# Optimization experiments

Measured on AMD Instinct MI355X. Metric: run time of the kernel, lower is better.

The kernel has to match this reference:

```python
import jax, jax.numpy as jnp
import numpy as np

ERR = 1e-12


def setup_inputs() -> dict:
    key = jax.random.key(0)
    k1, k2, k3 = jax.random.split(key, 3)
    B, H, L, D = 2, 16, 2048, 64
    k = jax.random.normal(k1, (B, H, L, D), dtype=jnp.float32)
    src = jax.random.uniform(k2, (B, H, L), dtype=jnp.float32)
    dest = jax.random.uniform(k3, (B, H, L), dtype=jnp.float32)
    return {"k": k, "src": src, "dest": dest}


def reference(k, src, dest):
    # k: [B,H,L,D], src/dest: [B,H,L]
    L = k.shape[-2]
    s = jnp.sqrt(src + ERR)   # sqrt-scaled source weights
    d = jnp.sqrt(dest + ERR)  # sqrt-scaled destination weights
    # affinity_1[b,h,i,j] = s_i * d_j * (k_i . k_j), fused as (k*s) @ (k*d)^T
    a1 = jnp.einsum("bhid,bhjd->bhij", k * s[..., :, None], k * d[..., :, None])
    # relu then (x+err)^(2/3)  (kernel: exp2(log2(relu(a)+err) * 2/3))
    a3 = jnp.exp2(jnp.log2(jax.nn.relu(a1) + ERR) * (2.0 / 3.0))
    # forward cumulative sum over j, output causally masked to j >= i
    cs = jnp.cumsum(a3, axis=-1)
    idx = jnp.arange(L)
    mask = idx[:, None] <= idx[None, :]  # keep j >= i
    return jnp.where(mask, cs, 0.0)
```

## Files before the change

### kernel.cpp

```cpp
#include <hip/hip_runtime.h>

#define BH   32
#define LSEQ 2048
#define DDIM 64
#define ERRC 1e-12f

typedef __attribute__((ext_vector_type(8)))  short bf16x8;
typedef __attribute__((ext_vector_type(4)))  float floatx4;
typedef __attribute__((ext_vector_type(4)))  unsigned short ushort4v;

__device__ __forceinline__ unsigned short f2bf(float f) {
    unsigned u = __float_as_uint(f);
    u = u + 0x7FFFu + ((u >> 16) & 1u);
    return (unsigned short)(u >> 16);
}

__device__ __forceinline__ bf16x8 pack8s(const float* __restrict__ p, float w) {
    const floatx4* pv = (const floatx4*)p;
    floatx4 x = pv[0], y = pv[1];
    bf16x8 r;
    r[0] = (short)f2bf(x[0] * w); r[1] = (short)f2bf(x[1] * w);
    r[2] = (short)f2bf(x[2] * w); r[3] = (short)f2bf(x[3] * w);
    r[4] = (short)f2bf(y[0] * w); r[5] = (short)f2bf(y[1] * w);
    r[6] = (short)f2bf(y[2] * w); r[7] = (short)f2bf(y[3] * w);
    return r;
}

__global__ __launch_bounds__(256) void prep_scaled(const float* __restrict__ k,
                                                   const float* __restrict__ src,
                                                   const float* __restrict__ dest,
                                                   unsigned short* __restrict__ ks,
                                                   unsigned short* __restrict__ kd) {
    int idx4 = blockIdx.x * 256 + threadIdx.x;
    int row  = idx4 >> 4;
    float s = sqrtf(src[row] + ERRC);
    float d = sqrtf(dest[row] + ERRC);
    floatx4 v = ((const floatx4*)k)[idx4];
    ushort4v os, od;
#pragma unroll
    for (int r = 0; r < 4; ++r) { os[r] = f2bf(v[r] * s); od[r] = f2bf(v[r] * d); }
    ((ushort4v*)ks)[idx4] = os;
    ((ushort4v*)kd)[idx4] = od;
}

template<bool RAW>
__device__ __forceinline__ void load_row16(const void* __restrict__ kp, long base, int row,
                                           int q, const float* __restrict__ w, int bhL,
                                           bf16x8& lo, bf16x8& hi) {
    if (RAW) {
        const float* p = (const float*)kp + base + (long)row * DDIM + q * 8;
        float s = sqrtf(w[bhL + row] + ERRC);
        lo = pack8s(p, s);
        hi = pack8s(p + 32, s);
    } else {
        const unsigned short* p = (const unsigned short*)kp + base + (long)row * DDIM + q * 8;
        lo = *(const bf16x8*)p;
        hi = *(const bf16x8*)(p + 32);
    }
}

template<bool RAW>
__global__ __launch_bounds__(256, 4) void mha_fused4(const void* __restrict__ ka,
                                                     const void* __restrict__ kb,
                                                     const float* __restrict__ src,
                                                     const float* __restrict__ dest,
                                                     float* __restrict__ out) {
    const int tid  = threadIdx.x;
    const int wave = tid >> 6;
    const int lane = tid & 63;
    const int q    = lane >> 4;
    const int l16  = lane & 15;
    const int bh = blockIdx.x & 31;
    const int ib = blockIdx.x >> 5;
    const int i0 = (ib * 4 + wave) * 16;
    const int bhL = bh * LSEQ;
    const long base = (long)bh * LSEQ * DDIM;

    bf16x8 blo, bhi;
    load_row16<RAW>(kb, base, i0 + l16, q, src, bhL, blo, bhi);

    float carry = 0.f;
    const float c23 = 2.0f / 3.0f;

    bf16x8 aLo[4], aHi[4];
#pragma unroll
    for (int t = 0; t < 4; ++t)
        load_row16<RAW>(ka, base, 16 * t + l16, q, dest, bhL, aLo[t], aHi[t]);

    float* orow = out + (long)(bhL + i0 + l16) * LSEQ + q * 4;

    for (int it = 0; it < 32; ++it) {
        const int j0 = it << 6;

        bf16x8 nLo[4], nHi[4];
        const int jn = (it < 31) ? (j0 + 64) : 0;
#pragma unroll
        for (int t = 0; t < 4; ++t)
            load_row16<RAW>(ka, base, jn + 16 * t + l16, q, dest, bhL, nLo[t], nHi[t]);

        floatx4 acc[4];
#pragma unroll
        for (int t = 0; t < 4; ++t) {
            floatx4 z = {0.f, 0.f, 0.f, 0.f};
            z = __builtin_amdgcn_mfma_f32_16x16x32_bf16(aLo[t], blo, z, 0, 0, 0);
            acc[t] = __builtin_amdgcn_mfma_f32_16x16x32_bf16(aHi[t], bhi, z, 0, 0, 0);
        }

        float u[4][4];
#pragma unroll
        for (int t = 0; t < 4; ++t)
#pragma unroll
            for (int r = 0; r < 4; ++r) {
                float v = fmaxf(acc[t][r], 0.f) + ERRC;
                u[t][r] = exp2f(c23 * __log2f(v));
            }

        if (j0 + 64 <= i0) {
            float s = 0.f;
#pragma unroll
            for (int t = 0; t < 4; ++t)
                s += (u[t][0] + u[t][1]) + (u[t][2] + u[t][3]);
            float s1 = s + __shfl_xor(s, 16, 64);
            carry += s1 + __shfl_xor(s1, 32, 64);
            const floatx4 z = {0.f, 0.f, 0.f, 0.f};
#pragma unroll
            for (int t = 0; t < 4; ++t)
                *(floatx4*)(orow + j0 + 16 * t) = z;
        } else {
#pragma unroll
            for (int t = 0; t < 4; ++t) {
                const int jt0 = j0 + 16 * t;
                if (jt0 + 16 <= i0) {
                    float s = (u[t][0] + u[t][1]) + (u[t][2] + u[t][3]);
                    float s1 = s + __shfl_xor(s, 16, 64);
                    carry += s1 + __shfl_xor(s1, 32, 64);
                    const floatx4 z = {0.f, 0.f, 0.f, 0.f};
                    *(floatx4*)(orow + jt0) = z;
                } else {
                    u[t][1] += u[t][0];
                    u[t][2] += u[t][1];
                    u[t][3] += u[t][2];
                    const float S   = u[t][3];
                    const float x16 = __shfl_xor(S, 16, 64);
                    const float s1  = S + x16;
                    const float x32 = __shfl_xor(s1, 32, 64);
                    const float E = ((q & 1) ? x16 : 0.f) + ((q & 2) ? x32 : 0.f) + carry;
                    carry += s1 + x32;
                    floatx4 o;
                    if (jt0 == i0) {
#pragma unroll
                        for (int r = 0; r < 4; ++r)
                            o[r] = ((q * 4 + r) >= l16) ? (u[t][r] + E) : 0.f;
                    } else {
#pragma unroll
                        for (int r = 0; r < 4; ++r)
                            o[r] = u[t][r] + E;
                    }
                    *(floatx4*)(orow + jt0) = o;
                }
            }
        }

#pragma unroll
        for (int t = 0; t < 4; ++t) { aLo[t] = nLo[t]; aHi[t] = nHi[t]; }
    }
}

extern "C" void kernel_launch(void* const* d_in, const int* in_sizes, int n_in,
                              void* d_out, int out_size, void* d_ws, size_t ws_size,
                              hipStream_t stream) {
    const float* k    = (const float*)d_in[0];
    const float* src  = (const float*)d_in[1];
    const float* dest = (const float*)d_in[2];
    float* out = (float*)d_out;

    const size_t half = (size_t)BH * LSEQ * DDIM * sizeof(unsigned short);
    if (ws_size >= 2 * half) {
        unsigned short* ks = (unsigned short*)d_ws;
        unsigned short* kd = (unsigned short*)((char*)d_ws + half);
        prep_scaled<<<dim3(4096), dim3(256), 0, stream>>>(k, src, dest, ks, kd);
        mha_fused4<false><<<dim3(1024), dim3(256), 0, stream>>>(kd, ks, src, dest, out);
    } else {
        mha_fused4<true><<<dim3(1024), dim3(256), 0, stream>>>(k, k, src, dest, out);
    }
}
```

Baseline: 625.3 us.

## Stage output strips in LDS for coalesced row-contiguous global stores

Each wave now writes its 16x128 output tile into a per-wave shared-memory strip, then stores it to global memory as full contiguous row segments. Before, every store instruction touched 64-byte pieces scattered across 16 rows. Strips that lie entirely in the masked region skip LDS and write zeros directly. The cost is extra LDS traffic, 33 KB of shared memory per block, and a padded row stride that is not 16-byte aligned, which may break the vector LDS accesses into narrower ones.

```diff
diff --git a/kernel.cpp b/kernel.cpp
--- a/kernel.cpp
+++ b/kernel.cpp
@@ -4,6 +4,7 @@
 #define LSEQ 2048
 #define DDIM 64
 #define ERRC 1e-12f
+#define SROW 129
 
 typedef __attribute__((ext_vector_type(8)))  short bf16x8;
 typedef __attribute__((ext_vector_type(4)))  float floatx4;
@@ -60,11 +61,12 @@
 }
 
 template<bool RAW>
-__global__ __launch_bounds__(256, 4) void mha_fused4(const void* __restrict__ ka,
+__global__ __launch_bounds__(256, 4) void mha_fused5(const void* __restrict__ ka,
                                                      const void* __restrict__ kb,
                                                      const float* __restrict__ src,
                                                      const float* __restrict__ dest,
                                                      float* __restrict__ out) {
+    __shared__ float strip[4][16 * SROW];
     const int tid  = threadIdx.x;
     const int wave = tid >> 6;
     const int lane = tid & 63;
@@ -75,6 +77,7 @@
     const int i0 = (ib * 4 + wave) * 16;
     const int bhL = bh * LSEQ;
     const long base = (long)bh * LSEQ * DDIM;
+    float* sw = strip[wave];
 
     bf16x8 blo, bhi;
     load_row16<RAW>(kb, base, i0 + l16, q, src, bhL, blo, bhi);
@@ -87,82 +90,109 @@
     for (int t = 0; t < 4; ++t)
         load_row16<RAW>(ka, base, 16 * t + l16, q, dest, bhL, aLo[t], aHi[t]);
 
-    float* orow = out + (long)(bhL + i0 + l16) * LSEQ + q * 4;
-
-    for (int it = 0; it < 32; ++it) {
-        const int j0 = it << 6;
-
-        bf16x8 nLo[4], nHi[4];
-        const int jn = (it < 31) ? (j0 + 64) : 0;
-#pragma unroll
-        for (int t = 0; t < 4; ++t)
-            load_row16<RAW>(ka, base, jn + 16 * t + l16, q, dest, bhL, nLo[t], nHi[t]);
-
-        floatx4 acc[4];
-#pragma unroll
-        for (int t = 0; t < 4; ++t) {
-            floatx4 z = {0.f, 0.f, 0.f, 0.f};
-            z = __builtin_amdgcn_mfma_f32_16x16x32_bf16(aLo[t], blo, z, 0, 0, 0);
-            acc[t] = __builtin_amdgcn_mfma_f32_16x16x32_bf16(aHi[t], bhi, z, 0, 0, 0);
-        }
-
-        float u[4][4];
-#pragma unroll
-        for (int t = 0; t < 4; ++t)
-#pragma unroll
-            for (int r = 0; r < 4; ++r) {
-                float v = fmaxf(acc[t][r], 0.f) + ERRC;
-                u[t][r] = exp2f(c23 * __log2f(v));
+    const int h2  = lane >> 5;
+    const int c32 = lane & 31;
+    float* obase = out + (long)(bhL + i0 + h2) * LSEQ + 4 * c32;
+    const int lrd = h2 * SROW + 4 * c32;
+
+    for (int sup = 0; sup < 16; ++sup) {
+        const int j0s = sup << 7;
+        const bool maskedStrip = (j0s + 128) <= i0;
+
+#pragma unroll
+        for (int half = 0; half < 2; ++half) {
+            const int j0 = j0s + (half << 6);
+            const int colbase = half << 6;
+
+            bf16x8 nLo[4], nHi[4];
+            const int jn = (j0 + 64 < LSEQ) ? (j0 + 64) : 0;
+#pragma unroll
+            for (int t = 0; t < 4; ++t)
+                load_row16<RAW>(ka, base, jn + 16 * t + l16, q, dest, bhL, nLo[t], nHi[t]);
+
+            floatx4 acc[4];
+#pragma unroll
+            for (int t = 0; t < 4; ++t) {
+                floatx4 z4 = {0.f, 0.f, 0.f, 0.f};
+                z4 = __builtin_amdgcn_mfma_f32_16x16x32_bf16(aLo[t], blo, z4, 0, 0, 0);
+                acc[t] = __builtin_amdgcn_mfma_f32_16x16x32_bf16(aHi[t], bhi, z4, 0, 0, 0);
             }
 
-        if (j0 + 64 <= i0) {
-            float s = 0.f;
+            float u[4][4];
 #pragma unroll
             for (int t = 0; t < 4; ++t)
-                s += (u[t][0] + u[t][1]) + (u[t][2] + u[t][3]);
-            float s1 = s + __shfl_xor(s, 16, 64);
-            carry += s1 + __shfl_xor(s1, 32, 64);
-            const floatx4 z = {0.f, 0.f, 0.f, 0.f};
-#pragma unroll
-            for (int t = 0; t < 4; ++t)
-                *(floatx4*)(orow + j0 + 16 * t) = z;
-        } else {
-#pragma unroll
-            for (int t = 0; t < 4; ++t) {
-                const int jt0 = j0 + 16 * t;
-                if (jt0 + 16 <= i0) {
-                    float s = (u[t][0] + u[t][1]) + (u[t][2] + u[t][3]);
-                    float s1 = s + __shfl_xor(s, 16, 64);
-                    carry += s1 + __shfl_xor(s1, 32, 64);
+#pragma unroll
+                for (int r = 0; r < 4; ++r) {
+                    float v = fmaxf(acc[t][r], 0.f) + ERRC;
+                    u[t][r] = exp2f(c23 * __log2f(v));
+                }
+
+            if (j0 + 64 <= i0) {
+                float s = 0.f;
+#pragma unroll
+                for (int t = 0; t < 4; ++t)
+                    s += (u[t][0] + u[t][1]) + (u[t][2] + u[t][3]);
+                float s1 = s + __shfl_xor(s, 16, 64);
+                carry += s1 + __shfl_xor(s1, 32, 64);
+                if (!maskedStrip) {
                     const floatx4 z = {0.f, 0.f, 0.f, 0.f};
-                    *(floatx4*)(orow + jt0) = z;
-                } else {
-                    u[t][1] += u[t][0];
-                    u[t][2] += u[t][1];
-                    u[t][3] += u[t][2];
-                    const float S   = u[t][3];
-                    const float x16 = __shfl_xor(S, 16, 64);
-                    const float s1  = S + x16;
-                    const float x32 = __shfl_xor(s1, 32, 64);
-                    const float E = ((q & 1) ? x16 : 0.f) + ((q & 2) ? x32 : 0.f) + carry;
-                    carry += s1 + x32;
-                    floatx4 o;
-                    if (jt0 == i0) {
-#pragma unroll
-                        for (int r = 0; r < 4; ++r)
-                            o[r] = ((q * 4 + r) >= l16) ? (u[t][r] + E) : 0.f;
+#pragma unroll
+                    for (int t = 0; t < 4; ++t)
+                        *(floatx4*)&sw[l16 * SROW + colbase + 16 * t + 4 * q] = z;
+                }
+            } else {
+#pragma unroll
+                for (int t = 0; t < 4; ++t) {
+                    const int jt0 = j0 + 16 * t;
+                    float* dst = &sw[l16 * SROW + colbase + 16 * t + 4 * q];
+                    if (jt0 + 16 <= i0) {
+                        float s = (u[t][0] + u[t][1]) + (u[t][2] + u[t][3]);
+                        float s1 = s + __shfl_xor(s, 16, 64);
+                        carry += s1 + __shfl_xor(s1, 32, 64);
+                        const floatx4 z = {0.f, 0.f, 0.f, 0.f};
+                        *(floatx4*)dst = z;
                     } else {
-#pragma unroll
-                        for (int r = 0; r < 4; ++r)
-                            o[r] = u[t][r] + E;
+                        u[t][1] += u[t][0];
+                        u[t][2] += u[t][1];
+                        u[t][3] += u[t][2];
+                        const float S   = u[t][3];
+                        const float x16 = __shfl_xor(S, 16, 64);
+                        const float s1  = S + x16;
+                        const float x32 = __shfl_xor(s1, 32, 64);
+                        const float E = ((q & 1) ? x16 : 0.f) + ((q & 2) ? x32 : 0.f) + carry;
+                        carry += s1 + x32;
+                        floatx4 o;
+                        if (jt0 == i0) {
+#pragma unroll
+                            for (int r = 0; r < 4; ++r)
+                                o[r] = ((q * 4 + r) >= l16) ? (u[t][r] + E) : 0.f;
+                        } else {
+#pragma unroll
+                            for (int r = 0; r < 4; ++r)
+                                o[r] = u[t][r] + E;
+                        }
+                        *(floatx4*)dst = o;
                     }
-                    *(floatx4*)(orow + jt0) = o;
                 }
             }
+
+#pragma unroll
+            for (int t = 0; t < 4; ++t) { aLo[t] = nLo[t]; aHi[t] = nHi[t]; }
         }
 
-#pragma unroll
-        for (int t = 0; t < 4; ++t) { aLo[t] = nLo[t]; aHi[t] = nHi[t]; }
+        float* og = obase + j0s;
+        if (maskedStrip) {
+            const floatx4 z = {0.f, 0.f, 0.f, 0.f};
+#pragma unroll
+            for (int s = 0; s < 8; ++s)
+                *(floatx4*)(og + (long)(2 * s) * LSEQ) = z;
+        } else {
+#pragma unroll
+            for (int s = 0; s < 8; ++s) {
+                floatx4 v = *(const floatx4*)&sw[lrd + 2 * s * SROW];
+                *(floatx4*)(og + (long)(2 * s) * LSEQ) = v;
+            }
+        }
     }
 }
 
@@ -179,8 +209,8 @@
         unsigned short* ks = (unsigned short*)d_ws;
         unsigned short* kd = (unsigned short*)((char*)d_ws + half);
         prep_scaled<<<dim3(4096), dim3(256), 0, stream>>>(k, src, dest, ks, kd);
-        mha_fused4<false><<<dim3(1024), dim3(256), 0, stream>>>(kd, ks, src, dest, out);
+        mha_fused5<false><<<dim3(1024), dim3(256), 0, stream>>>(kd, ks, src, dest, out);
     } else {
-        mha_fused4<true><<<dim3(1024), dim3(256), 0, stream>>>(k, k, src, dest, out);
+        mha_fused5<true><<<dim3(1024), dim3(256), 0, stream>>>(k, k, src, dest, out);
     }
 }
```

Measured after the change: 613.5 us. No clear change (-1.9%).

## Split row scan into strip-sum pass plus parallel column-chunk output kernel

Applied to the files above, without the earlier changes.

The single fused kernel, where each wave scanned a full 2048-column row, is replaced by two passes. The first pass computes partial sums of the activated affinity over the first three 512-column chunks per row. The second pass launches per-chunk blocks that seed their carry from those sums, which gives more parallelism. It also stages outputs in LDS so each row is stored with coalesced, row-contiguous writes. The cost is recomputing the affinity for the first three quarters of columns, plus one extra launch and an extra workspace buffer.

```diff
diff --git a/kernel.cpp b/kernel.cpp
--- a/kernel.cpp
+++ b/kernel.cpp
@@ -4,6 +4,7 @@
 #define LSEQ 2048
 #define DDIM 64
 #define ERRC 1e-12f
+#define SROW2 260
 
 typedef __attribute__((ext_vector_type(8)))  short bf16x8;
 typedef __attribute__((ext_vector_type(4)))  float floatx4;
@@ -43,28 +44,228 @@
     ((ushort4v*)kd)[idx4] = od;
 }
 
-template<bool RAW>
-__device__ __forceinline__ void load_row16(const void* __restrict__ kp, long base, int row,
-                                           int q, const float* __restrict__ w, int bhL,
-                                           bf16x8& lo, bf16x8& hi) {
-    if (RAW) {
-        const float* p = (const float*)kp + base + (long)row * DDIM + q * 8;
-        float s = sqrtf(w[bhL + row] + ERRC);
-        lo = pack8s(p, s);
-        hi = pack8s(p + 32, s);
-    } else {
-        const unsigned short* p = (const unsigned short*)kp + base + (long)row * DDIM + q * 8;
-        lo = *(const bf16x8*)p;
-        hi = *(const bf16x8*)(p + 32);
-    }
-}
-
-template<bool RAW>
-__global__ __launch_bounds__(256, 4) void mha_fused4(const void* __restrict__ ka,
-                                                     const void* __restrict__ kb,
-                                                     const float* __restrict__ src,
-                                                     const float* __restrict__ dest,
-                                                     float* __restrict__ out) {
+__device__ __forceinline__ void load_frag(const unsigned short* __restrict__ p,
+                                          bf16x8& lo, bf16x8& hi) {
+    lo = *(const bf16x8*)p;
+    hi = *(const bf16x8*)(p + 32);
+}
+
+__global__ __launch_bounds__(256, 4) void strip_sums(const unsigned short* __restrict__ kd,
+                                                     const unsigned short* __restrict__ ks,
+                                                     float* __restrict__ S) {
+    const int tid  = threadIdx.x;
+    const int wave = tid >> 6;
+    const int lane = tid & 63;
+    const int q    = lane >> 4;
+    const int l16  = lane & 15;
+    const int bh   = blockIdx.x & 31;
+    const int ib   = blockIdx.x >> 5;
+    const int i0   = (ib * 4 + wave) * 16;
+    const int bhL  = bh * LSEQ;
+    const unsigned short* kdb = kd + (long)bh * LSEQ * DDIM;
+    const unsigned short* ksb = ks + (long)bh * LSEQ * DDIM;
+
+    bf16x8 blo, bhi;
+    load_frag(ksb + (long)(i0 + l16) * DDIM + q * 8, blo, bhi);
+
+    bf16x8 aLo[4], aHi[4];
+#pragma unroll
+    for (int t = 0; t < 4; ++t)
+        load_frag(kdb + (long)(16 * t + l16) * DDIM + q * 8, aLo[t], aHi[t]);
+
+    const float c23 = 2.0f / 3.0f;
+    float ssv[3];
+
+    for (int cc = 0; cc < 3; ++cc) {
+        float ss = 0.f;
+        for (int g = 0; g < 8; ++g) {
+            const int jn = (cc * 8 + g < 23) ? (cc * 512 + g * 64 + 64) : 0;
+            bf16x8 nLo[4], nHi[4];
+#pragma unroll
+            for (int t = 0; t < 4; ++t)
+                load_frag(kdb + (long)(jn + 16 * t + l16) * DDIM + q * 8, nLo[t], nHi[t]);
+
+            floatx4 acc[4];
+#pragma unroll
+            for (int t = 0; t < 4; ++t) {
+                floatx4 z4 = {0.f, 0.f, 0.f, 0.f};
+                z4 = __builtin_amdgcn_mfma_f32_16x16x32_bf16(aLo[t], blo, z4, 0, 0, 0);
+                acc[t] = __builtin_amdgcn_mfma_f32_16x16x32_bf16(aHi[t], bhi, z4, 0, 0, 0);
+            }
+
+            float s = 0.f;
+#pragma unroll
+            for (int t = 0; t < 4; ++t)
+#pragma unroll
+                for (int r = 0; r < 4; ++r) {
+                    float v = fmaxf(acc[t][r], 0.f) + ERRC;
+                    s += exp2f(c23 * __log2f(v));
+                }
+            float s1 = s + __shfl_xor(s, 16, 64);
+            ss += s1 + __shfl_xor(s1, 32, 64);
+
+#pragma unroll
+            for (int t = 0; t < 4; ++t) { aLo[t] = nLo[t]; aHi[t] = nHi[t]; }
+        }
+        ssv[cc] = ss;
+    }
+
+    float sv = (q == 0) ? ssv[0] : (q == 1) ? ssv[1] : ssv[2];
+    if (q < 3)
+        S[(long)(bhL + i0 + l16) * 4 + q] = sv;
+}
+
+__global__ __launch_bounds__(128, 2) void chunk_out(const unsigned short* __restrict__ kd,
+                                                    const unsigned short* __restrict__ ks,
+                                                    const float* __restrict__ S,
+                                                    float* __restrict__ out) {
+    __shared__ float strip[2][16 * SROW2];
+    const int tid  = threadIdx.x;
+    const int wave = tid >> 6;
+    const int lane = tid & 63;
+    const int q    = lane >> 4;
+    const int l16  = lane & 15;
+    const int bh   = blockIdx.x & 31;
+    const int rr   = blockIdx.x >> 5;
+    const int ib2  = rr & 63;
+    const int c    = rr >> 6;
+    const int i0   = (ib2 * 2 + wave) * 16;
+    const int bhL  = bh * LSEQ;
+    const int jb   = c << 9;
+
+    if (jb + 512 <= i0) {
+        const floatx4 z = {0.f, 0.f, 0.f, 0.f};
+#pragma unroll
+        for (int s = 0; s < 16; ++s) {
+            float* row = out + (long)(bhL + i0 + s) * LSEQ + jb + 4 * lane;
+            *(floatx4*)row = z;
+            *(floatx4*)(row + 256) = z;
+        }
+        return;
+    }
+
+    const unsigned short* kdb = kd + (long)bh * LSEQ * DDIM;
+    const unsigned short* ksb = ks + (long)bh * LSEQ * DDIM;
+    float* sw = strip[wave];
+
+    bf16x8 blo, bhi;
+    load_frag(ksb + (long)(i0 + l16) * DDIM + q * 8, blo, bhi);
+
+    float carry = 0.f;
+    const float* Sr = S + (long)(bhL + i0 + l16) * 4;
+#pragma unroll
+    for (int cc = 0; cc < 3; ++cc)
+        if (cc < c) carry += Sr[cc];
+
+    const float c23 = 2.0f / 3.0f;
+
+    bf16x8 aLo[4], aHi[4];
+#pragma unroll
+    for (int t = 0; t < 4; ++t)
+        load_frag(kdb + (long)(jb + 16 * t + l16) * DDIM + q * 8, aLo[t], aHi[t]);
+
+    for (int hh = 0; hh < 2; ++hh) {
+#pragma unroll
+        for (int gg = 0; gg < 4; ++gg) {
+            const int colbase = gg * 64;
+            const int j0 = jb + hh * 256 + colbase;
+            const int jl = hh * 256 + colbase + 64;
+            const int jn = jb + ((jl < 512) ? jl : 0);
+
+            bf16x8 nLo[4], nHi[4];
+#pragma unroll
+            for (int t = 0; t < 4; ++t)
+                load_frag(kdb + (long)(jn + 16 * t + l16) * DDIM + q * 8, nLo[t], nHi[t]);
+
+            floatx4 acc[4];
+#pragma unroll
+            for (int t = 0; t < 4; ++t) {
+                floatx4 z4 = {0.f, 0.f, 0.f, 0.f};
+                z4 = __builtin_amdgcn_mfma_f32_16x16x32_bf16(aLo[t], blo, z4, 0, 0, 0);
+                acc[t] = __builtin_amdgcn_mfma_f32_16x16x32_bf16(aHi[t], bhi, z4, 0, 0, 0);
+            }
+
+            float u[4][4];
+#pragma unroll
+            for (int t = 0; t < 4; ++t)
+#pragma unroll
+                for (int r = 0; r < 4; ++r) {
+                    float v = fmaxf(acc[t][r], 0.f) + ERRC;
+                    u[t][r] = exp2f(c23 * __log2f(v));
+                }
+
+            if (j0 + 64 <= i0) {
+                float s = 0.f;
+#pragma unroll
+                for (int t = 0; t < 4; ++t)
+                    s += (u[t][0] + u[t][1]) + (u[t][2] + u[t][3]);
+                float s1 = s + __shfl_xor(s, 16, 64);
+                carry += s1 + __shfl_xor(s1, 32, 64);
+                const floatx4 z = {0.f, 0.f, 0.f, 0.f};
+#pragma unroll
+                for (int t = 0; t < 4; ++t)
+                    *(floatx4*)&sw[l16 * SROW2 + colbase + 16 * t + 4 * q] = z;
+            } else {
+#pragma unroll
+                for (int t = 0; t < 4; ++t) {
+                    const int jt0 = j0 + 16 * t;
+                    float* dst = &sw[l16 * SROW2 + colbase + 16 * t + 4 * q];
+                    if (jt0 + 16 <= i0) {
+                        float s = (u[t][0] + u[t][1]) + (u[t][2] + u[t][3]);
+                        float s1 = s + __shfl_xor(s, 16, 64);
+                        carry += s1 + __shfl_xor(s1, 32, 64);
+                        const floatx4 z = {0.f, 0.f, 0.f, 0.f};
+                        *(floatx4*)dst = z;
+                    } else {
+                        u[t][1] += u[t][0];
+                        u[t][2] += u[t][1];
+                        u[t][3] += u[t][2];
+                        const float Sg  = u[t][3];
+                        const float x16 = __shfl_xor(Sg, 16, 64);
+                        const float s1  = Sg + x16;
+                        const float x32 = __shfl_xor(s1, 32, 64);
+                        const float E = ((q & 1) ? x16 : 0.f) + ((q & 2) ? x32 : 0.f) + carry;
+                        carry += s1 + x32;
+                        floatx4 o;
+                        if (jt0 == i0) {
+#pragma unroll
+                            for (int r = 0; r < 4; ++r)
+                                o[r] = ((q * 4 + r) >= l16) ? (u[t][r] + E) : 0.f;
+                        } else {
+#pragma unroll
+                            for (int r = 0; r < 4; ++r)
+                                o[r] = u[t][r] + E;
+                        }
+                        *(floatx4*)dst = o;
+                    }
+                }
+            }
+
+#pragma unroll
+            for (int t = 0; t < 4; ++t) { aLo[t] = nLo[t]; aHi[t] = nHi[t]; }
+        }
+
+#pragma unroll
+        for (int s = 0; s < 16; ++s) {
+            floatx4 v = *(const floatx4*)&sw[s * SROW2 + 4 * lane];
+            *(floatx4*)(out + (long)(bhL + i0 + s) * LSEQ + jb + hh * 256 + 4 * lane) = v;
+        }
+    }
+}
+
+__device__ __forceinline__ void load_row16_raw(const float* __restrict__ kp, long base, int row,
+                                               int q, const float* __restrict__ w, int bhL,
+                                               bf16x8& lo, bf16x8& hi) {
+    const float* p = kp + base + (long)row * DDIM + q * 8;
+    float s = sqrtf(w[bhL + row] + ERRC);
+    lo = pack8s(p, s);
+    hi = pack8s(p + 32, s);
+}
+
+__global__ __launch_bounds__(256, 4) void mha_raw(const float* __restrict__ kp,
+                                                  const float* __restrict__ src,
+                                                  const float* __restrict__ dest,
+                                                  float* __restrict__ out) {
     const int tid  = threadIdx.x;
     const int wave = tid >> 6;
     const int lane = tid & 63;
@@ -77,7 +278,7 @@
     const long base = (long)bh * LSEQ * DDIM;
 
     bf16x8 blo, bhi;
-    load_row16<RAW>(kb, base, i0 + l16, q, src, bhL, blo, bhi);
+    load_row16_raw(kp, base, i0 + l16, q, src, bhL, blo, bhi);
 
     float carry = 0.f;
     const float c23 = 2.0f / 3.0f;
@@ -85,25 +286,24 @@
     bf16x8 aLo[4], aHi[4];
 #pragma unroll
     for (int t = 0; t < 4; ++t)
-        load_row16<RAW>(ka, base, 16 * t + l16, q, dest, bhL, aLo[t], aHi[t]);
+        load_row16_raw(kp, base, 16 * t + l16, q, dest, bhL, aLo[t], aHi[t]);
 
     float* orow = out + (long)(bhL + i0 + l16) * LSEQ + q * 4;
 
     for (int it = 0; it < 32; ++it) {
         const int j0 = it << 6;
-
         bf16x8 nLo[4], nHi[4];
         const int jn = (it < 31) ? (j0 + 64) : 0;
 #pragma unroll
         for (int t = 0; t < 4; ++t)
-            load_row16<RAW>(ka, base, jn + 16 * t + l16, q, dest, bhL, nLo[t], nHi[t]);
+            load_row16_raw(kp, base, jn + 16 * t + l16, q, dest, bhL, nLo[t], nHi[t]);
 
         floatx4 acc[4];
 #pragma unroll
         for (int t = 0; t < 4; ++t) {
-            floatx4 z = {0.f, 0.f, 0.f, 0.f};
-            z = __builtin_amdgcn_mfma_f32_16x16x32_bf16(aLo[t], blo, z, 0, 0, 0);
-            acc[t] = __builtin_amdgcn_mfma_f32_16x16x32_bf16(aHi[t], bhi, z, 0, 0, 0);
+            floatx4 z4 = {0.f, 0.f, 0.f, 0.f};
+            z4 = __builtin_amdgcn_mfma_f32_16x16x32_bf16(aLo[t], blo, z4, 0, 0, 0);
+            acc[t] = __builtin_amdgcn_mfma_f32_16x16x32_bf16(aHi[t], bhi, z4, 0, 0, 0);
         }
 
         float u[4][4];
@@ -115,49 +315,36 @@
                 u[t][r] = exp2f(c23 * __log2f(v));
             }
 
-        if (j0 + 64 <= i0) {
-            float s = 0.f;
-#pragma unroll
-            for (int t = 0; t < 4; ++t)
-                s += (u[t][0] + u[t][1]) + (u[t][2] + u[t][3]);
-            float s1 = s + __shfl_xor(s, 16, 64);
-            carry += s1 + __shfl_xor(s1, 32, 64);
-            const floatx4 z = {0.f, 0.f, 0.f, 0.f};
-#pragma unroll
-            for (int t = 0; t < 4; ++t)
-                *(floatx4*)(orow + j0 + 16 * t) = z;
-        } else {
-#pragma unroll
-            for (int t = 0; t < 4; ++t) {
-                const int jt0 = j0 + 16 * t;
-                if (jt0 + 16 <= i0) {
-                    float s = (u[t][0] + u[t][1]) + (u[t][2] + u[t][3]);
-                    float s1 = s + __shfl_xor(s, 16, 64);
-                    carry += s1 + __shfl_xor(s1, 32, 64);
-                    const floatx4 z = {0.f, 0.f, 0.f, 0.f};
-                    *(floatx4*)(orow + jt0) = z;
+#pragma unroll
+        for (int t = 0; t < 4; ++t) {
+            const int jt0 = j0 + 16 * t;
+            if (jt0 + 16 <= i0) {
+                float s = (u[t][0] + u[t][1]) + (u[t][2] + u[t][3]);
+                float s1 = s + __shfl_xor(s, 16, 64);
+                carry += s1 + __shfl_xor(s1, 32, 64);
+                const floatx4 z = {0.f, 0.f, 0.f, 0.f};
+                *(floatx4*)(orow + jt0) = z;
+            } else {
+                u[t][1] += u[t][0];
+                u[t][2] += u[t][1];
+                u[t][3] += u[t][2];
+                const float Sg  = u[t][3];
+                const float x16 = __shfl_xor(Sg, 16, 64);
+                const float s1  = Sg + x16;
+                const float x32 = __shfl_xor(s1, 32, 64);
+                const float E = ((q & 1) ? x16 : 0.f) + ((q & 2) ? x32 : 0.f) + carry;
+                carry += s1 + x32;
+                floatx4 o;
+                if (jt0 == i0) {
+#pragma unroll
+                    for (int r = 0; r < 4; ++r)
+                        o[r] = ((q * 4 + r) >= l16) ? (u[t][r] + E) : 0.f;
                 } else {
-                    u[t][1] += u[t][0];
-                    u[t][2] += u[t][1];
-                    u[t][3] += u[t][2];
-                    const float S   = u[t][3];
-                    const float x16 = __shfl_xor(S, 16, 64);
-                    const float s1  = S + x16;
-                    const float x32 = __shfl_xor(s1, 32, 64);
-                    const float E = ((q & 1) ? x16 : 0.f) + ((q & 2) ? x32 : 0.f) + carry;
-                    carry += s1 + x32;
-                    floatx4 o;
-                    if (jt0 == i0) {
-#pragma unroll
-                        for (int r = 0; r < 4; ++r)
-                            o[r] = ((q * 4 + r) >= l16) ? (u[t][r] + E) : 0.f;
-                    } else {
-#pragma unroll
-                        for (int r = 0; r < 4; ++r)
-                            o[r] = u[t][r] + E;
-                    }
-                    *(floatx4*)(orow + jt0) = o;
+#pragma unroll
+                    for (int r = 0; r < 4; ++r)
+                        o[r] = u[t][r] + E;
                 }
+                *(floatx4*)(orow + jt0) = o;
             }
         }
 
@@ -175,12 +362,15 @@
     float* out = (float*)d_out;
 
     const size_t half = (size_t)BH * LSEQ * DDIM * sizeof(unsigned short);
-    if (ws_size >= 2 * half) {
+    const size_t ssz  = (size_t)BH * LSEQ * 4 * sizeof(float);
+    if (ws_size >= 2 * half + ssz) {
         unsigned short* ks = (unsigned short*)d_ws;
         unsigned short* kd = (unsigned short*)((char*)d_ws + half);
+        float* S = (float*)((char*)d_ws + 2 * half);
         prep_scaled<<<dim3(4096), dim3(256), 0, stream>>>(k, src, dest, ks, kd);
-        mha_fused4<false><<<dim3(1024), dim3(256), 0, stream>>>(kd, ks, src, dest, out);
+        strip_sums<<<dim3(1024), dim3(256), 0, stream>>>(kd, ks, S);
+        chunk_out<<<dim3(8192), dim3(128), 0, stream>>>(kd, ks, S, out);
     } else {
-        mha_fused4<true><<<dim3(1024), dim3(256), 0, stream>>>(k, k, src, dest, out);
-    }
-}
+        mha_raw<<<dim3(1024), dim3(256), 0, stream>>>(k, src, dest, out);
+    }
+}
```

After: 684.6 us. +9.5%, slower.

## Stage key tiles through LDS with async global_load_lds and fragment-ordered layout

Applied to the files above, without the earlier changes.

The prep kernel now writes the dest-scaled keys in an MFMA-fragment-ordered tiled layout. The main kernel stages each 64-row key tile into a double-buffered LDS region using direct global-to-LDS loads, so the four waves of a block share one copy instead of each fetching the tile into registers. This reduces redundant global/L2 traffic and register pressure for the prefetch. It adds a block barrier per iteration, which couples the waves and may stall those doing causal prefix work. The kernel is write-bound on the large output, so the benefit may be small.

```diff
diff --git a/kernel.cpp b/kernel.cpp
--- a/kernel.cpp
+++ b/kernel.cpp
@@ -26,45 +26,39 @@
     return r;
 }
 
-__global__ __launch_bounds__(256) void prep_scaled(const float* __restrict__ k,
-                                                   const float* __restrict__ src,
-                                                   const float* __restrict__ dest,
-                                                   unsigned short* __restrict__ ks,
-                                                   unsigned short* __restrict__ kd) {
+__global__ __launch_bounds__(256) void prep_scaled2(const float* __restrict__ k,
+                                                    const float* __restrict__ src,
+                                                    const float* __restrict__ dest,
+                                                    unsigned short* __restrict__ ks,
+                                                    unsigned short* __restrict__ kd) {
     int idx4 = blockIdx.x * 256 + threadIdx.x;
     int row  = idx4 >> 4;
+    int d    = (idx4 & 15) * 4;
     float s = sqrtf(src[row] + ERRC);
-    float d = sqrtf(dest[row] + ERRC);
+    float dd = sqrtf(dest[row] + ERRC);
     floatx4 v = ((const floatx4*)k)[idx4];
     ushort4v os, od;
 #pragma unroll
-    for (int r = 0; r < 4; ++r) { os[r] = f2bf(v[r] * s); od[r] = f2bf(v[r] * d); }
+    for (int r = 0; r < 4; ++r) { os[r] = f2bf(v[r] * s); od[r] = f2bf(v[r] * dd); }
     ((ushort4v*)ks)[idx4] = os;
-    ((ushort4v*)kd)[idx4] = od;
-}
-
-template<bool RAW>
-__device__ __forceinline__ void load_row16(const void* __restrict__ kp, long base, int row,
-                                           int q, const float* __restrict__ w, int bhL,
-                                           bf16x8& lo, bf16x8& hi) {
-    if (RAW) {
-        const float* p = (const float*)kp + base + (long)row * DDIM + q * 8;
-        float s = sqrtf(w[bhL + row] + ERRC);
-        lo = pack8s(p, s);
-        hi = pack8s(p + 32, s);
-    } else {
-        const unsigned short* p = (const unsigned short*)kp + base + (long)row * DDIM + q * 8;
-        lo = *(const bf16x8*)p;
-        hi = *(const bf16x8*)(p + 32);
-    }
-}
-
-template<bool RAW>
-__global__ __launch_bounds__(256, 4) void mha_fused4(const void* __restrict__ ka,
-                                                     const void* __restrict__ kb,
-                                                     const float* __restrict__ src,
-                                                     const float* __restrict__ dest,
+    const int jt   = row >> 4;
+    const int l16  = row & 15;
+    const int half = d >> 5;
+    const int q    = (d & 31) >> 3;
+    const long off = (long)jt * 1024 + half * 512 + (q * 16 + l16) * 8 + (d & 7);
+    *(ushort4v*)(kd + off) = od;
+}
+
+__device__ __forceinline__ void gll16(const unsigned short* g, unsigned short* l) {
+    __builtin_amdgcn_global_load_lds(
+        (const __attribute__((address_space(1))) unsigned int*)(const void*)g,
+        (__attribute__((address_space(3))) unsigned int*)(void*)l, 16, 0, 0);
+}
+
+__global__ __launch_bounds__(256, 4) void mha_fused9(const unsigned short* __restrict__ kdt,
+                                                     const unsigned short* __restrict__ ks,
                                                      float* __restrict__ out) {
+    __shared__ __align__(16) unsigned short stage[2][4096];
     const int tid  = threadIdx.x;
     const int wave = tid >> 6;
     const int lane = tid & 63;
@@ -74,36 +68,45 @@
     const int ib = blockIdx.x >> 5;
     const int i0 = (ib * 4 + wave) * 16;
     const int bhL = bh * LSEQ;
-    const long base = (long)bh * LSEQ * DDIM;
-
-    bf16x8 blo, bhi;
-    load_row16<RAW>(kb, base, i0 + l16, q, src, bhL, blo, bhi);
+    const unsigned short* kdb = kdt + (long)bh * (128 * 1024);
+
+    const unsigned short* bp = ks + (long)(bhL + i0 + l16) * DDIM + q * 8;
+    const bf16x8 blo = *(const bf16x8*)bp;
+    const bf16x8 bhi = *(const bf16x8*)(bp + 32);
 
     float carry = 0.f;
     const float c23 = 2.0f / 3.0f;
-
-    bf16x8 aLo[4], aHi[4];
-#pragma unroll
-    for (int t = 0; t < 4; ++t)
-        load_row16<RAW>(ka, base, 16 * t + l16, q, dest, bhL, aLo[t], aHi[t]);
-
     float* orow = out + (long)(bhL + i0 + l16) * LSEQ + q * 4;
 
-    for (int it = 0; it < 32; ++it) {
-        const int j0 = it << 6;
-
-        bf16x8 nLo[4], nHi[4];
-        const int jn = (it < 31) ? (j0 + 64) : 0;
-#pragma unroll
-        for (int t = 0; t < 4; ++t)
-            load_row16<RAW>(ka, base, jn + 16 * t + l16, q, dest, bhL, nLo[t], nHi[t]);
+    {
+        const unsigned short* g0 = kdb + wave * 1024 + lane * 8;
+        unsigned short* l0 = &stage[0][wave * 1024];
+        gll16(g0, l0);
+        gll16(g0 + 512, l0 + 512);
+    }
+    __syncthreads();
+
+    int cur = 0;
+    for (int g = 0; g < 32; ++g) {
+        const int j0 = g << 6;
+
+        const int gn = (g < 31) ? (g + 1) : 0;
+        {
+            const unsigned short* gs = kdb + (long)(gn * 4 + wave) * 1024 + lane * 8;
+            unsigned short* ld = &stage[cur ^ 1][wave * 1024];
+            gll16(gs, ld);
+            gll16(gs + 512, ld + 512);
+        }
 
         floatx4 acc[4];
 #pragma unroll
         for (int t = 0; t < 4; ++t) {
-            floatx4 z = {0.f, 0.f, 0.f, 0.f};
-            z = __builtin_amdgcn_mfma_f32_16x16x32_bf16(aLo[t], blo, z, 0, 0, 0);
-            acc[t] = __builtin_amdgcn_mfma_f32_16x16x32_bf16(aHi[t], bhi, z, 0, 0, 0);
+            const unsigned short* tb = &stage[cur][t * 1024 + lane * 8];
+            bf16x8 alo = *(const bf16x8*)tb;
+            bf16x8 ahi = *(const bf16x8*)(tb + 512);
+            floatx4 z4 = {0.f, 0.f, 0.f, 0.f};
+            z4 = __builtin_amdgcn_mfma_f32_16x16x32_bf16(alo, blo, z4, 0, 0, 0);
+            acc[t] = __builtin_amdgcn_mfma_f32_16x16x32_bf16(ahi, bhi, z4, 0, 0, 0);
         }
 
         float u[4][4];
@@ -140,9 +143,9 @@
                     u[t][1] += u[t][0];
                     u[t][2] += u[t][1];
                     u[t][3] += u[t][2];
-                    const float S   = u[t][3];
-                    const float x16 = __shfl_xor(S, 16, 64);
-                    const float s1  = S + x16;
+                    const float Sg  = u[t][3];
+                    const float x16 = __shfl_xor(Sg, 16, 64);
+                    const float s1  = Sg + x16;
                     const float x32 = __shfl_xor(s1, 32, 64);
                     const float E = ((q & 1) ? x16 : 0.f) + ((q & 2) ? x32 : 0.f) + carry;
                     carry += s1 + x32;
@@ -158,6 +161,106 @@
                     }
                     *(floatx4*)(orow + jt0) = o;
                 }
+            }
+        }
+
+        __syncthreads();
+        cur ^= 1;
+    }
+}
+
+__device__ __forceinline__ void load_row16_raw(const float* __restrict__ kp, long base, int row,
+                                               int q, const float* __restrict__ w, int bhL,
+                                               bf16x8& lo, bf16x8& hi) {
+    const float* p = kp + base + (long)row * DDIM + q * 8;
+    float s = sqrtf(w[bhL + row] + ERRC);
+    lo = pack8s(p, s);
+    hi = pack8s(p + 32, s);
+}
+
+__global__ __launch_bounds__(256, 4) void mha_raw(const float* __restrict__ kp,
+                                                  const float* __restrict__ src,
+                                                  const float* __restrict__ dest,
+                                                  float* __restrict__ out) {
+    const int tid  = threadIdx.x;
+    const int wave = tid >> 6;
+    const int lane = tid & 63;
+    const int q    = lane >> 4;
+    const int l16  = lane & 15;
+    const int bh = blockIdx.x & 31;
+    const int ib = blockIdx.x >> 5;
+    const int i0 = (ib * 4 + wave) * 16;
+    const int bhL = bh * LSEQ;
+    const long base = (long)bh * LSEQ * DDIM;
+
+    bf16x8 blo, bhi;
+    load_row16_raw(kp, base, i0 + l16, q, src, bhL, blo, bhi);
+
+    float carry = 0.f;
+    const float c23 = 2.0f / 3.0f;
+
+    bf16x8 aLo[4], aHi[4];
+#pragma unroll
+    for (int t = 0; t < 4; ++t)
+        load_row16_raw(kp, base, 16 * t + l16, q, dest, bhL, aLo[t], aHi[t]);
+
+    float* orow = out + (long)(bhL + i0 + l16) * LSEQ + q * 4;
+
+    for (int it = 0; it < 32; ++it) {
+        const int j0 = it << 6;
+        bf16x8 nLo[4], nHi[4];
+        const int jn = (it < 31) ? (j0 + 64) : 0;
+#pragma unroll
+        for (int t = 0; t < 4; ++t)
+            load_row16_raw(kp, base, jn + 16 * t + l16, q, dest, bhL, nLo[t], nHi[t]);
+
+        floatx4 acc[4];
+#pragma unroll
+        for (int t = 0; t < 4; ++t) {
+            floatx4 z4 = {0.f, 0.f, 0.f, 0.f};
+            z4 = __builtin_amdgcn_mfma_f32_16x16x32_bf16(aLo[t], blo, z4, 0, 0, 0);
+            acc[t] = __builtin_amdgcn_mfma_f32_16x16x32_bf16(aHi[t], bhi, z4, 0, 0, 0);
+        }
+
+        float uu[4][4];
+#pragma unroll
+        for (int t = 0; t < 4; ++t)
+#pragma unroll
+            for (int r = 0; r < 4; ++r) {
+                float v = fmaxf(acc[t][r], 0.f) + ERRC;
+                uu[t][r] = exp2f(c23 * __log2f(v));
+            }
+
+#pragma unroll
+        for (int t = 0; t < 4; ++t) {
+            const int jt0 = j0 + 16 * t;
+            if (jt0 + 16 <= i0) {
+                float s = (uu[t][0] + uu[t][1]) + (uu[t][2] + uu[t][3]);
+                float s1 = s + __shfl_xor(s, 16, 64);
+                carry += s1 + __shfl_xor(s1, 32, 64);
+                const floatx4 z = {0.f, 0.f, 0.f, 0.f};
+                *(floatx4*)(orow + jt0) = z;
+            } else {
+                uu[t][1] += uu[t][0];
+                uu[t][2] += uu[t][1];
+                uu[t][3] += uu[t][2];
+                const float Sg  = uu[t][3];
+                const float x16 = __shfl_xor(Sg, 16, 64);
+                const float s1  = Sg + x16;
+                const float x32 = __shfl_xor(s1, 32, 64);
+                const float E = ((q & 1) ? x16 : 0.f) + ((q & 2) ? x32 : 0.f) + carry;
+                carry += s1 + x32;
+                floatx4 o;
+                if (jt0 == i0) {
+#pragma unroll
+                    for (int r = 0; r < 4; ++r)
+                        o[r] = ((q * 4 + r) >= l16) ? (uu[t][r] + E) : 0.f;
+                } else {
+#pragma unroll
+                    for (int r = 0; r < 4; ++r)
+                        o[r] = uu[t][r] + E;
+                }
+                *(floatx4*)(orow + jt0) = o;
             }
         }
 
@@ -178,9 +281,9 @@
     if (ws_size >= 2 * half) {
         unsigned short* ks = (unsigned short*)d_ws;
         unsigned short* kd = (unsigned short*)((char*)d_ws + half);
-        prep_scaled<<<dim3(4096), dim3(256), 0, stream>>>(k, src, dest, ks, kd);
-        mha_fused4<false><<<dim3(1024), dim3(256), 0, stream>>>(kd, ks, src, dest, out);
+        prep_scaled2<<<dim3(4096), dim3(256), 0, stream>>>(k, src, dest, ks, kd);
+        mha_fused9<<<dim3(1024), dim3(256), 0, stream>>>(kd, ks, out);
     } else {
-        mha_fused4<true><<<dim3(1024), dim3(256), 0, stream>>>(k, k, src, dest, out);
-    }
-}
+        mha_raw<<<dim3(1024), dim3(256), 0, stream>>>(k, src, dest, out);
+    }
+}
```

Result: faster. 584.8 us (-6.5%).
